# Kernel tuning notes

Measured on AMD Instinct MI355X. Metric: run time of the kernel, lower is better.

Reference implementation:

```python
import jax, jax.numpy as jnp
import numpy as np

CHUNK = 512  # points per scan step; keeps per-step (B,CHUNK,M) dist tile ~64MB

def _nn_min_sqdist(x, y):
    """Per-point squared distance to nearest neighbor.
    x: (B,N,3), y: (B,M,3) -> (B,N). Chunked over N to avoid a full (B,N,M) matrix.
    """
    B, N, D = x.shape
    y2 = jnp.sum(y * y, axis=-1)  # (B,M)
    nchunks = N // CHUNK
    xc = x.reshape(B, nchunks, CHUNK, D).transpose(1, 0, 2, 3)  # (nchunks,B,C,D)

    def body(carry, xck):  # xck: (B,C,D)
        x2 = jnp.sum(xck * xck, axis=-1)  # (B,C)
        d = x2[:, :, None] + y2[:, None, :] - 2.0 * jnp.einsum('bcd,bmd->bcm', xck, y)
        return carry, jnp.min(d, axis=-1)  # (B,C)

    _, mins = jax.lax.scan(body, None, xc)  # (nchunks,B,C)
    return mins.transpose(1, 0, 2).reshape(B, N)


def setup_inputs() -> dict:
    key = jax.random.key(0)
    k1, k2 = jax.random.split(key)
    pred = jax.random.normal(k1, (4, 8192, 3), dtype=jnp.float32)
    gt = jax.random.normal(k2, (4, 8192, 3), dtype=jnp.float32)
    return {"pred": pred, "gt": gt}


def reference(pred, gt):
    beta, gamma, delta = 1.0, 1.0, 0.0  # ChamferLoss defaults; threshold=None, percentage=1.0
    N = pred.shape[1]
    pred2gt = _nn_min_sqdist(pred, gt)  # (B,N)
    gt2pred = _nn_min_sqdist(gt, pred)  # (B,M)
    loss = (jnp.mean(pred2gt, axis=-1)
            + jnp.mean(gt2pred, axis=-1) * (delta * N + gamma)
            + jnp.max(pred2gt, axis=-1) * beta)
    return jnp.mean(loss)
```

## Files before the change

kernel.cpp:

```cpp
#include <hip/hip_runtime.h>


typedef short  s16x8  __attribute__((ext_vector_type(8)));
typedef float  f32x16 __attribute__((ext_vector_type(16)));

#define BATCH 4
#define NPTS  8192
#define TPB   256
#define YS    4
#define YPS   (NPTS / YS)
#define STPTS 1024
#define STTILES (STPTS / 32)
#define XPB   256
#define NXC   (NPTS / XPB)
#define RBLK  64

__device__ __forceinline__ unsigned int bft(float f) { return __float_as_uint(f) >> 16; }
__device__ __forceinline__ float bfv(unsigned int s) { return __uint_as_float(s << 16); }

__device__ __forceinline__ void yfrag(float a0, float a1, float a2,
                                      uint4& w0, uint4& w1) {
    const unsigned int yh0 = bft(a0), yh1 = bft(a1), yh2 = bft(a2);
    const float l0 = a0 - bfv(yh0), l1 = a1 - bfv(yh1), l2 = a2 - bfv(yh2);
    const unsigned int nh0 = bft(-2.f * bfv(yh0));
    const unsigned int nh1 = bft(-2.f * bfv(yh1));
    const unsigned int nh2 = bft(-2.f * bfv(yh2));
    const unsigned int nl0 = bft(-2.f * l0), nl1 = bft(-2.f * l1), nl2 = bft(-2.f * l2);
    const float y2 = a0 * a0 + a1 * a1 + a2 * a2;
    const unsigned int q2h = bft(y2);
    const unsigned int q2l = bft(y2 - bfv(q2h));
    w0.x = nh0 | (nh1 << 16);
    w0.y = nh2 | (nl0 << 16);
    w0.z = nl1 | (nl2 << 16);
    w0.w = nh0 | (nh1 << 16);
    w1.x = nh2 | (q2h << 16);
    w1.y = q2l;
    w1.z = 0u; w1.w = 0u;
}

__global__ __launch_bounds__(TPB, 4)
void nn_fused(const float* __restrict__ pred, const float* __restrict__ gt,
              float* __restrict__ pmin, unsigned int* __restrict__ accum) {
    const int xc = blockIdx.x, sl = blockIdx.y, bd = blockIdx.z;
    const int t = threadIdx.x;
    if (xc == 0 && sl == 0 && bd == 0 && t < 17) accum[t] = 0u;

    const int b = bd >> 1, dir = bd & 1;
    const float* xp = (dir ? gt : pred) + (size_t)b * NPTS * 3;
    const float* yp = (dir ? pred : gt) + (size_t)b * NPTS * 3;

    const int w = t >> 6, l = t & 63;
    const int m32 = l & 31, hh = l >> 5;
    const int xbase = xc * XPB + w * 64;

    __shared__ uint4 ldsb[STTILES * 64];

    s16x8 af[2];
    float x2j[2];
    #pragma unroll
    for (int j = 0; j < 2; ++j) {
        const int xi = xbase + j * 32 + m32;
        const float c0 = xp[xi * 3], c1 = xp[xi * 3 + 1], c2 = xp[xi * 3 + 2];
        x2j[j] = c0 * c0 + c1 * c1 + c2 * c2;
        const unsigned int xh0 = bft(c0), xh1 = bft(c1), xh2 = bft(c2);
        const unsigned int xl0 = bft(c0 - bfv(xh0));
        const unsigned int xl1 = bft(c1 - bfv(xh1));
        const unsigned int xl2 = bft(c2 - bfv(xh2));
        s16x8 a;
        a[0] = (short)(hh ? xl2 : xh0);
        a[1] = (short)(hh ? 0x3F80u : xh1);
        a[2] = (short)(hh ? 0x3F80u : xh2);
        a[3] = (short)(hh ? 0u : xh0);
        a[4] = (short)(hh ? 0u : xh1);
        a[5] = (short)(hh ? 0u : xh2);
        a[6] = (short)(hh ? 0u : xl0);
        a[7] = (short)(hh ? 0u : xl1);
        af[j] = a;
    }

    f32x16 zero, mn0, mn1;
    #pragma unroll
    for (int r = 0; r < 16; ++r) { zero[r] = 0.f; mn0[r] = 3.4e38f; mn1[r] = 3.4e38f; }

    const uint4* bp = ldsb + l;

    for (int s = 0; s < 2; ++s) {
        if (s) __syncthreads();
        #pragma unroll
        for (int i = 0; i < 4; ++i) {
            const int p = i * 256 + t;
            const int pt = sl * YPS + s * STPTS + p;
            const float a0 = yp[pt * 3], a1 = yp[pt * 3 + 1], a2 = yp[pt * 3 + 2];
            uint4 q0, q1;
            yfrag(a0, a1, a2, q0, q1);
            ldsb[(p >> 5) * 64 + (p & 31)]      = q0;
            ldsb[(p >> 5) * 64 + 32 + (p & 31)] = q1;
        }
        __syncthreads();
        #pragma unroll
        for (int tp = 0; tp < STTILES; tp += 2) {
            const s16x8 bfa = __builtin_bit_cast(s16x8, bp[tp * 64]);
            const s16x8 bfb = __builtin_bit_cast(s16x8, bp[(tp + 1) * 64]);
            {
                const f32x16 e0a = __builtin_amdgcn_mfma_f32_32x32x16_bf16(af[0], bfa, zero, 0, 0, 0);
                const f32x16 e0b = __builtin_amdgcn_mfma_f32_32x32x16_bf16(af[0], bfb, zero, 0, 0, 0);
                #pragma unroll
                for (int r = 0; r < 16; ++r)
                    mn0[r] = fminf(fminf(mn0[r], e0a[r]), e0b[r]);
            }
            {
                const f32x16 e1a = __builtin_amdgcn_mfma_f32_32x32x16_bf16(af[1], bfa, zero, 0, 0, 0);
                const f32x16 e1b = __builtin_amdgcn_mfma_f32_32x32x16_bf16(af[1], bfb, zero, 0, 0, 0);
                #pragma unroll
                for (int r = 0; r < 16; ++r)
                    mn1[r] = fminf(fminf(mn1[r], e1a[r]), e1b[r]);
            }
        }
    }

    #pragma unroll
    for (int off = 16; off; off >>= 1) {
        #pragma unroll
        for (int r = 0; r < 16; ++r) {
            mn0[r] = fminf(mn0[r], __shfl_xor(mn0[r], off, 64));
            mn1[r] = fminf(mn1[r], __shfl_xor(mn1[r], off, 64));
        }
    }

    const int r = l & 15;
    const int row = (r & 3) + 8 * (r >> 2) + 4 * hh;
    float v0 = mn0[0], v1 = mn1[0];
    #pragma unroll
    for (int rr = 1; rr < 16; ++rr) {
        v0 = (r == rr) ? mn0[rr] : v0;
        v1 = (r == rr) ? mn1[rr] : v1;
    }
    const float x20 = __shfl(x2j[0], row, 64);
    const float x21 = __shfl(x2j[1], row, 64);
    const bool g1 = (l & 31) >= 16;
    const float d = fmaxf((g1 ? v1 : v0) + (g1 ? x21 : x20), 0.f);
    const int xpt = xbase + (g1 ? 32 : 0) + row;
    pmin[((size_t)bd * YS + sl) * NPTS + xpt] = d;
}

__global__ __launch_bounds__(TPB)
void reduce_all(const float* __restrict__ pmin, float* __restrict__ accum,
                float* __restrict__ out) {
    const int g = blockIdx.x, bd = g >> 3, seg = g & 7;
    const int t = threadIdx.x;
    const float4* base = (const float4*)(pmin + (size_t)bd * YS * NPTS);
    const int f4 = seg * 256 + t;
    float4 q = base[f4];
    #pragma unroll
    for (int sl = 1; sl < YS; ++sl) {
        const float4 rr = base[sl * (NPTS / 4) + f4];
        q.x = fminf(q.x, rr.x); q.y = fminf(q.y, rr.y);
        q.z = fminf(q.z, rr.z); q.w = fminf(q.w, rr.w);
    }
    float s = (q.x + q.y) + (q.z + q.w);
    float m = fmaxf(fmaxf(q.x, q.y), fmaxf(q.z, q.w));
    #pragma unroll
    for (int off = 32; off; off >>= 1) {
        s += __shfl_down(s, off, 64);
        m = fmaxf(m, __shfl_down(m, off, 64));
    }
    __shared__ float ws_[4], wm_[4];
    if ((t & 63) == 0) { ws_[t >> 6] = s; wm_[t >> 6] = m; }
    __syncthreads();
    if (t == 0) {
        s = (ws_[0] + ws_[1]) + (ws_[2] + ws_[3]);
        m = fmaxf(fmaxf(wm_[0], wm_[1]), fmaxf(wm_[2], wm_[3]));
        atomicAdd(&accum[bd], s);
        atomicMax((unsigned int*)accum + 8 + bd, __float_as_uint(m));
        __threadfence();
        const unsigned int done = atomicAdd((unsigned int*)accum + 16, 1u);
        if (done == RBLK - 1) {
            float acc = 0.f;
            #pragma unroll
            for (int b2 = 0; b2 < BATCH; ++b2) {
                const float s0 = atomicAdd(&accum[2 * b2], 0.f);
                const float s1 = atomicAdd(&accum[2 * b2 + 1], 0.f);
                const unsigned int mb =
                    atomicMax((unsigned int*)accum + 8 + 2 * b2, 0u);
                acc += (s0 + s1) * (1.f / NPTS) + __uint_as_float(mb);
            }
            out[0] = acc * (1.f / BATCH);
        }
    }
}

extern "C" void kernel_launch(void* const* d_in, const int* in_sizes, int n_in,
                              void* d_out, int out_size, void* d_ws, size_t ws_size,
                              hipStream_t stream) {
    const float* pred = (const float*)d_in[0];
    const float* gt   = (const float*)d_in[1];

    float* pmin = (float*)d_ws;
    float* accum = (float*)((char*)d_ws + (size_t)2 * BATCH * YS * NPTS * 4);

    dim3 g1(NXC, YS, 2 * BATCH);
    nn_fused<<<g1, TPB, 0, stream>>>(pred, gt, pmin, (unsigned int*)accum);
    reduce_all<<<dim3(RBLK), TPB, 0, stream>>>(pmin, accum, (float*)d_out);
}
```

Baseline: 82.14 us.

## Use 512-thread blocks with one x-fragment per wave and two y slices

The nearest-neighbor kernel now uses 512-thread blocks where each wave handles 32 x points with a single A fragment, instead of 64 points with two fragments. The y dimension is split into 2 slices instead of 4, and each slice is staged through 64KB of LDS in two 2048-point phases. This halves the partial-min buffer and the reduction reads, and it spreads the x work over more waves. In exchange, each LDS B-fragment read now feeds half as many MFMAs, the larger LDS footprint may cap occupancy, and half the lanes sit idle at the store.

```diff
diff --git a/kernel.cpp b/kernel.cpp
--- a/kernel.cpp
+++ b/kernel.cpp
@@ -6,37 +6,18 @@
 
 #define BATCH 4
 #define NPTS  8192
-#define TPB   256
-#define YS    4
-#define YPS   (NPTS / YS)
-#define STPTS 1024
-#define STTILES (STPTS / 32)
+#define TPB   512
 #define XPB   256
 #define NXC   (NPTS / XPB)
+#define YS    2
+#define YPS   (NPTS / YS)
+#define PHPTS 2048
+#define NPH   (YPS / PHPTS)
+#define PHT   (PHPTS / 32)
 #define RBLK  64
 
 __device__ __forceinline__ unsigned int bft(float f) { return __float_as_uint(f) >> 16; }
 __device__ __forceinline__ float bfv(unsigned int s) { return __uint_as_float(s << 16); }
-
-__device__ __forceinline__ void yfrag(float a0, float a1, float a2,
-                                      uint4& w0, uint4& w1) {
-    const unsigned int yh0 = bft(a0), yh1 = bft(a1), yh2 = bft(a2);
-    const float l0 = a0 - bfv(yh0), l1 = a1 - bfv(yh1), l2 = a2 - bfv(yh2);
-    const unsigned int nh0 = bft(-2.f * bfv(yh0));
-    const unsigned int nh1 = bft(-2.f * bfv(yh1));
-    const unsigned int nh2 = bft(-2.f * bfv(yh2));
-    const unsigned int nl0 = bft(-2.f * l0), nl1 = bft(-2.f * l1), nl2 = bft(-2.f * l2);
-    const float y2 = a0 * a0 + a1 * a1 + a2 * a2;
-    const unsigned int q2h = bft(y2);
-    const unsigned int q2l = bft(y2 - bfv(q2h));
-    w0.x = nh0 | (nh1 << 16);
-    w0.y = nh2 | (nl0 << 16);
-    w0.z = nl1 | (nl2 << 16);
-    w0.w = nh0 | (nh1 << 16);
-    w1.x = nh2 | (q2h << 16);
-    w1.y = q2l;
-    w1.z = 0u; w1.w = 0u;
-}
 
 __global__ __launch_bounds__(TPB, 4)
 void nn_fused(const float* __restrict__ pred, const float* __restrict__ gt,
@@ -49,101 +30,96 @@
     const float* xp = (dir ? gt : pred) + (size_t)b * NPTS * 3;
     const float* yp = (dir ? pred : gt) + (size_t)b * NPTS * 3;
 
-    const int w = t >> 6, l = t & 63;
+    const int wv = t >> 6, l = t & 63;
     const int m32 = l & 31, hh = l >> 5;
-    const int xbase = xc * XPB + w * 64;
 
-    __shared__ uint4 ldsb[STTILES * 64];
+    __shared__ uint4 ldsb[PHT * 64];
 
-    s16x8 af[2];
-    float x2j[2];
-    #pragma unroll
-    for (int j = 0; j < 2; ++j) {
-        const int xi = xbase + j * 32 + m32;
-        const float c0 = xp[xi * 3], c1 = xp[xi * 3 + 1], c2 = xp[xi * 3 + 2];
-        x2j[j] = c0 * c0 + c1 * c1 + c2 * c2;
+    const int xi = xc * XPB + wv * 32 + m32;
+    const float c0 = xp[xi * 3], c1 = xp[xi * 3 + 1], c2 = xp[xi * 3 + 2];
+    const float x2 = c0 * c0 + c1 * c1 + c2 * c2;
+    s16x8 af;
+    {
         const unsigned int xh0 = bft(c0), xh1 = bft(c1), xh2 = bft(c2);
         const unsigned int xl0 = bft(c0 - bfv(xh0));
         const unsigned int xl1 = bft(c1 - bfv(xh1));
         const unsigned int xl2 = bft(c2 - bfv(xh2));
-        s16x8 a;
-        a[0] = (short)(hh ? xl2 : xh0);
-        a[1] = (short)(hh ? 0x3F80u : xh1);
-        a[2] = (short)(hh ? 0x3F80u : xh2);
-        a[3] = (short)(hh ? 0u : xh0);
-        a[4] = (short)(hh ? 0u : xh1);
-        a[5] = (short)(hh ? 0u : xh2);
-        a[6] = (short)(hh ? 0u : xl0);
-        a[7] = (short)(hh ? 0u : xl1);
-        af[j] = a;
+        af[0] = (short)(hh ? xl2 : xh0);
+        af[1] = (short)(hh ? 0x3F80u : xh1);
+        af[2] = (short)(hh ? 0x3F80u : xh2);
+        af[3] = (short)(hh ? 0u : xh0);
+        af[4] = (short)(hh ? 0u : xh1);
+        af[5] = (short)(hh ? 0u : xh2);
+        af[6] = (short)(hh ? 0u : xl0);
+        af[7] = (short)(hh ? 0u : xl1);
     }
 
-    f32x16 zero, mn0, mn1;
+    f32x16 zero, mn;
     #pragma unroll
-    for (int r = 0; r < 16; ++r) { zero[r] = 0.f; mn0[r] = 3.4e38f; mn1[r] = 3.4e38f; }
+    for (int r = 0; r < 16; ++r) { zero[r] = 0.f; mn[r] = 3.4e38f; }
 
     const uint4* bp = ldsb + l;
 
-    for (int s = 0; s < 2; ++s) {
-        if (s) __syncthreads();
+    for (int ph = 0; ph < NPH; ++ph) {
+        if (ph) __syncthreads();
         #pragma unroll
-        for (int i = 0; i < 4; ++i) {
-            const int p = i * 256 + t;
-            const int pt = sl * YPS + s * STPTS + p;
+        for (int i = 0; i < PHPTS / TPB; ++i) {
+            const int q = i * TPB + t;
+            const int pt = sl * YPS + ph * PHPTS + q;
             const float a0 = yp[pt * 3], a1 = yp[pt * 3 + 1], a2 = yp[pt * 3 + 2];
-            uint4 q0, q1;
-            yfrag(a0, a1, a2, q0, q1);
-            ldsb[(p >> 5) * 64 + (p & 31)]      = q0;
-            ldsb[(p >> 5) * 64 + 32 + (p & 31)] = q1;
+            const unsigned int yh0 = bft(a0), yh1 = bft(a1), yh2 = bft(a2);
+            const float l0 = a0 - bfv(yh0), l1 = a1 - bfv(yh1), l2 = a2 - bfv(yh2);
+            const unsigned int nh0 = bft(-2.f * bfv(yh0));
+            const unsigned int nh1 = bft(-2.f * bfv(yh1));
+            const unsigned int nh2 = bft(-2.f * bfv(yh2));
+            const unsigned int nl0 = bft(-2.f * l0), nl1 = bft(-2.f * l1), nl2 = bft(-2.f * l2);
+            const float y2 = a0 * a0 + a1 * a1 + a2 * a2;
+            const unsigned int q2h = bft(y2);
+            const unsigned int q2l = bft(y2 - bfv(q2h));
+            uint4 w0, w1;
+            w0.x = nh0 | (nh1 << 16);
+            w0.y = nh2 | (nl0 << 16);
+            w0.z = nl1 | (nl2 << 16);
+            w0.w = nh0 | (nh1 << 16);
+            w1.x = nh2 | (q2h << 16);
+            w1.y = q2l;
+            w1.z = 0u; w1.w = 0u;
+            ldsb[(q >> 5) * 64 + (q & 31)]      = w0;
+            ldsb[(q >> 5) * 64 + 32 + (q & 31)] = w1;
         }
         __syncthreads();
-        #pragma unroll
-        for (int tp = 0; tp < STTILES; tp += 2) {
-            const s16x8 bfa = __builtin_bit_cast(s16x8, bp[tp * 64]);
-            const s16x8 bfb = __builtin_bit_cast(s16x8, bp[(tp + 1) * 64]);
-            {
-                const f32x16 e0a = __builtin_amdgcn_mfma_f32_32x32x16_bf16(af[0], bfa, zero, 0, 0, 0);
-                const f32x16 e0b = __builtin_amdgcn_mfma_f32_32x32x16_bf16(af[0], bfb, zero, 0, 0, 0);
-                #pragma unroll
-                for (int r = 0; r < 16; ++r)
-                    mn0[r] = fminf(fminf(mn0[r], e0a[r]), e0b[r]);
-            }
-            {
-                const f32x16 e1a = __builtin_amdgcn_mfma_f32_32x32x16_bf16(af[1], bfa, zero, 0, 0, 0);
-                const f32x16 e1b = __builtin_amdgcn_mfma_f32_32x32x16_bf16(af[1], bfb, zero, 0, 0, 0);
-                #pragma unroll
-                for (int r = 0; r < 16; ++r)
-                    mn1[r] = fminf(fminf(mn1[r], e1a[r]), e1b[r]);
-            }
+
+        for (int i = 0; i < PHT; i += 2) {
+            const s16x8 b0 = __builtin_bit_cast(s16x8, bp[i * 64]);
+            const s16x8 b1 = __builtin_bit_cast(s16x8, bp[(i + 1) * 64]);
+            const f32x16 e0 = __builtin_amdgcn_mfma_f32_32x32x16_bf16(af, b0, zero, 0, 0, 0);
+            const f32x16 e1 = __builtin_amdgcn_mfma_f32_32x32x16_bf16(af, b1, zero, 0, 0, 0);
+            #pragma unroll
+            for (int r = 0; r < 16; ++r)
+                mn[r] = fminf(fminf(mn[r], e0[r]), e1[r]);
         }
     }
 
     #pragma unroll
-    for (int off = 16; off; off >>= 1) {
+    for (int off = 16; off; off >>= 1)
         #pragma unroll
-        for (int r = 0; r < 16; ++r) {
-            mn0[r] = fminf(mn0[r], __shfl_xor(mn0[r], off, 64));
-            mn1[r] = fminf(mn1[r], __shfl_xor(mn1[r], off, 64));
-        }
-    }
+        for (int r = 0; r < 16; ++r)
+            mn[r] = fminf(mn[r], __shfl_xor(mn[r], off, 64));
 
     const int r = l & 15;
     const int row = (r & 3) + 8 * (r >> 2) + 4 * hh;
-    float v0 = mn0[0], v1 = mn1[0];
+    float v = mn[0];
     #pragma unroll
-    for (int rr = 1; rr < 16; ++rr) {
-        v0 = (r == rr) ? mn0[rr] : v0;
-        v1 = (r == rr) ? mn1[rr] : v1;
+    for (int rr = 1; rr < 16; ++rr) v = (r == rr) ? mn[rr] : v;
+    const float x2s = __shfl(x2, row, 64);
+    if ((l & 31) < 16) {
+        const float d = fmaxf(v + x2s, 0.f);
+        const int xpt = xc * XPB + wv * 32 + row;
+        pmin[((size_t)bd * YS + sl) * NPTS + xpt] = d;
     }
-    const float x20 = __shfl(x2j[0], row, 64);
-    const float x21 = __shfl(x2j[1], row, 64);
-    const bool g1 = (l & 31) >= 16;
-    const float d = fmaxf((g1 ? v1 : v0) + (g1 ? x21 : x20), 0.f);
-    const int xpt = xbase + (g1 ? 32 : 0) + row;
-    pmin[((size_t)bd * YS + sl) * NPTS + xpt] = d;
 }
 
-__global__ __launch_bounds__(TPB)
+__global__ __launch_bounds__(256)
 void reduce_all(const float* __restrict__ pmin, float* __restrict__ accum,
                 float* __restrict__ out) {
     const int g = blockIdx.x, bd = g >> 3, seg = g & 7;
@@ -200,5 +176,5 @@
 
     dim3 g1(NXC, YS, 2 * BATCH);
     nn_fused<<<g1, TPB, 0, stream>>>(pred, gt, pmin, (unsigned int*)accum);
-    reduce_all<<<dim3(RBLK), TPB, 0, stream>>>(pmin, accum, (float*)d_out);
+    reduce_all<<<dim3(RBLK), 256, 0, stream>>>(pmin, accum, (float*)d_out);
 }
```

After: 81.29 us. Within noise of the previous version (-1.0%).
